# Optimization experiments

Hardware: AMD Instinct MI355X
Metric: run time of the kernel (lower is better)

Reference implementation:

```python
import jax, jax.numpy as jnp
import numpy as np

EMBED_DIM = 1024
NUM_HEADS = 16
HEAD_DIM = EMBED_DIM // NUM_HEADS
QUANTUM_HEADS = 2
BATCH = 2
SEQ = 2048


def setup_inputs() -> dict:
    key = jax.random.key(0)
    ks = jax.random.split(key, 12)
    s = 1.0 / np.sqrt(EMBED_DIM)
    d = {
        "x": jax.random.normal(ks[0], (BATCH, SEQ, EMBED_DIM), jnp.float32),
        "Wq": jax.random.normal(ks[1], (EMBED_DIM, EMBED_DIM), jnp.float32) * s,
        "bq": jax.random.normal(ks[2], (EMBED_DIM,), jnp.float32) * s,
        "Wk": jax.random.normal(ks[3], (EMBED_DIM, EMBED_DIM), jnp.float32) * s,
        "bk": jax.random.normal(ks[4], (EMBED_DIM,), jnp.float32) * s,
        "Wv": jax.random.normal(ks[5], (EMBED_DIM, EMBED_DIM), jnp.float32) * s,
        "bv": jax.random.normal(ks[6], (EMBED_DIM,), jnp.float32) * s,
        "Wo": jax.random.normal(ks[7], (EMBED_DIM, EMBED_DIM), jnp.float32) * s,
        "bo": jax.random.normal(ks[8], (EMBED_DIM,), jnp.float32) * s,
        # surrogate params for the per-head quantum expectation layers
        "qw": jax.random.normal(ks[9], (QUANTUM_HEADS,), jnp.float32),
        "qb": jax.random.normal(ks[10], (QUANTUM_HEADS,), jnp.float32) * 0.1,
    }
    return d


def reference(x, Wq, bq, Wk, bk, Wv, bv, Wo, bo, qw, qb):
    B, S, E = x.shape
    H, D, QH = NUM_HEADS, HEAD_DIM, QUANTUM_HEADS

    def proj(W, b):  # nn.Linear: x @ W.T + b, then split heads -> (B,H,S,D)
        y = jnp.einsum("bse,fe->bsf", x, W) + b
        return y.reshape(B, S, H, D).transpose(0, 2, 1, 3)

    q = proj(Wq, bq)
    k = proj(Wk, bk)
    v = proj(Wv, bv)

    scores = jnp.einsum("bhsd,bhtd->bhst", q, k) / jnp.sqrt(jnp.float32(D))
    attn = jax.nn.softmax(scores, axis=-1)  # (B,H,S,S)

    # quantum-head post-softmax rescaling: per (batch, quantum head) scalar
    agg = attn[:, :QH].mean(axis=(2, 3))            # (B,QH)
    refined = jnp.cos(qw[None, :] * agg + qb[None, :])  # surrogate expectation in [-1,1]
    scale = jnp.concatenate(
        [refined, jnp.ones((B, H - QH), dtype=attn.dtype)], axis=1
    )  # (B,H)
    attn = attn * scale[:, :, None, None]

    out = jnp.einsum("bhst,bhtd->bhsd", attn, v)
    out = out.transpose(0, 2, 1, 3).reshape(B, S, E)
    out = jnp.einsum("bse,fe->bsf", out, Wo) + bo
    return out
```

## Files before the change

### kernel.cpp

```cpp
#include <hip/hip_runtime.h>
#include <hip/hip_bf16.h>

#define B_ 2
#define S_ 2048
#define E_ 1024
#define H_ 16
#define D_ 64

typedef __attribute__((ext_vector_type(8))) short short8;
typedef __attribute__((ext_vector_type(4))) float f32x4;
typedef __attribute__((ext_vector_type(16))) float f32x16;
typedef __attribute__((ext_vector_type(4))) unsigned short u16x4;

#define AS1 __attribute__((address_space(1)))
#define AS3 __attribute__((address_space(3)))

static __device__ __forceinline__ unsigned short f2bf(float f) {
  unsigned int u = __builtin_bit_cast(unsigned int, f);
  return (unsigned short)((u + 0x7fffu + ((u >> 16) & 1u)) >> 16);
}
static __device__ __forceinline__ unsigned short f2bf_f(float f) {
  unsigned int u = __builtin_bit_cast(unsigned int, f);
  return (unsigned short)((u + 0x8000u) >> 16);
}
static __device__ __forceinline__ void gload_lds16(const void* g, void* l) {
  __builtin_amdgcn_global_load_lds((const AS1 unsigned int*)g, (AS3 unsigned int*)l, 16, 0, 0);
}

__global__ __launch_bounds__(256) void cvt_all(const float* __restrict__ x,
                                               const float* __restrict__ w0,
                                               const float* __restrict__ w1,
                                               const float* __restrict__ w2,
                                               const float* __restrict__ w3,
                                               unsigned short* __restrict__ xb,
                                               unsigned short* __restrict__ wcat) {
  const int y = blockIdx.y;
  const float* src;
  unsigned short* dst;
  if (y < 4) {
    src = (y == 0) ? w0 : (y == 1) ? w1 : (y == 2) ? w2 : w3;
    dst = wcat + (size_t)y * (E_ * E_);
  } else {
    src = x + (size_t)(y - 4) * (E_ * E_);
    dst = xb + (size_t)(y - 4) * (E_ * E_);
  }
  int i = blockIdx.x * 1024 + threadIdx.x * 4;
  f32x4 v = *(const f32x4*)(src + i);
  u16x4 o;
  o.x = f2bf(v.x); o.y = f2bf(v.y); o.z = f2bf(v.z); o.w = f2bf(v.w);
  *(u16x4*)(dst + i) = o;
}

__global__ __launch_bounds__(256) void gemm_qkv3(const unsigned short* __restrict__ A,
                                                 const unsigned short* __restrict__ W,
                                                 const float* __restrict__ bq,
                                                 const float* __restrict__ bk,
                                                 const float* __restrict__ bv,
                                                 unsigned short* __restrict__ Qo,
                                                 unsigned short* __restrict__ Ko,
                                                 unsigned short* __restrict__ VT) {
  __shared__ __align__(16) unsigned short sm[128 * 64 * 2];
  unsigned short* lA = sm;
  unsigned short* lB = sm + 128 * 64;
  const int K = E_;
  const int tid  = threadIdx.x;
  const int lane = tid & 63;
  const int w    = tid >> 6;
  const int wm   = (w >> 1) * 64, wn = (w & 1) * 64;
  const int li   = lane & 15, quad = lane >> 4;
  const int e7   = li & 7;
  const int m0   = blockIdx.x * 128, n0 = blockIdx.y * 128;

  f32x4 acc[4][4];
#pragma unroll
  for (int i = 0; i < 4; ++i)
#pragma unroll
    for (int j = 0; j < 4; ++j) { f32x4 z = {0.f, 0.f, 0.f, 0.f}; acc[i][j] = z; }

  const unsigned short* pA[4];
  const unsigned short* pB[4];
#pragma unroll
  for (int q = 0; q < 4; ++q) {
    int p = tid + 256 * q, row = p >> 3, kc = (p & 7) ^ (row & 7);
    pA[q] = A + (size_t)(m0 + row) * K + kc * 8;
    pB[q] = W + (size_t)(n0 + row) * K + kc * 8;
  }

  for (int k0 = 0; k0 < K; k0 += 64) {
    __syncthreads();
#pragma unroll
    for (int q = 0; q < 4; ++q) gload_lds16(pA[q] + k0, &lA[(tid + 256 * q) * 8]);
#pragma unroll
    for (int q = 0; q < 4; ++q) gload_lds16(pB[q] + k0, &lB[(tid + 256 * q) * 8]);
    __syncthreads();
#pragma unroll
    for (int ks = 0; ks < 2; ++ks) {
      short8 af[4], bf[4];
#pragma unroll
      for (int i = 0; i < 4; ++i)
        af[i] = *(const short8*)&lA[(wm + i * 16 + li) * 64 + (((ks * 4 + quad) ^ e7) << 3)];
#pragma unroll
      for (int j = 0; j < 4; ++j)
        bf[j] = *(const short8*)&lB[(wn + j * 16 + li) * 64 + (((ks * 4 + quad) ^ e7) << 3)];
#pragma unroll
      for (int i = 0; i < 4; ++i)
#pragma unroll
        for (int j = 0; j < 4; ++j)
          acc[i][j] = __builtin_amdgcn_mfma_f32_16x16x32_bf16(af[i], bf[j], acc[i][j], 0, 0, 0);
    }
  }

  const int third = blockIdx.y >> 3;
  if (third < 2) {
    unsigned short* C = (third == 0) ? Qo : Ko;
    const float* bias = (third == 0) ? bq : bk;
    const float sc = (third == 0) ? 0.125f : 1.0f;
#pragma unroll
    for (int j = 0; j < 4; ++j) {
      int colf = (n0 & 1023) + wn + j * 16 + li;
      float bvv = bias[colf];
#pragma unroll
      for (int i = 0; i < 4; ++i)
#pragma unroll
        for (int r = 0; r < 4; ++r) {
          int row = m0 + wm + i * 16 + quad * 4 + r;
          C[(size_t)row * E_ + colf] = f2bf_f((acc[i][j][r] + bvv) * sc);
        }
    }
  } else {
    const int base = (blockIdx.y & 7) * 128;
    __syncthreads();
#pragma unroll
    for (int j = 0; j < 4; ++j) {
      int col = wn + j * 16 + li;
      float bvv = bv[base + col];
      int cm15 = col & 15;
#pragma unroll
      for (int i = 0; i < 4; ++i) {
        int s = wm + i * 16 + quad * 4;
        int off = col * 128 + (((s >> 3) ^ cm15) << 3) + (s & 7);
        u16x4 o;
        o.x = f2bf_f(acc[i][j][0] + bvv);
        o.y = f2bf_f(acc[i][j][1] + bvv);
        o.z = f2bf_f(acc[i][j][2] + bvv);
        o.w = f2bf_f(acc[i][j][3] + bvv);
        *(u16x4*)&sm[off] = o;
      }
    }
    __syncthreads();
    int col = tid >> 1, half = tid & 1;
    int colf = base + col;
    int h2 = colf >> 6, d2 = colf & 63;
    int bb = m0 >> 11, s2 = m0 & 2047;
    unsigned short* dst = VT + (((size_t)bb * 16 + h2) * 64 + d2) * 2048 + s2 + half * 64;
    int cm15 = col & 15;
#pragma unroll
    for (int u = 0; u < 8; ++u) {
      int sc2 = half * 8 + u;
      *(short8*)(dst + u * 8) = *(const short8*)&sm[col * 128 + ((sc2 ^ cm15) << 3)];
    }
  }
}

__global__ __launch_bounds__(256) void gemm_out64(const unsigned short* __restrict__ A,
                                                  const unsigned short* __restrict__ W,
                                                  const float* __restrict__ bias,
                                                  float* __restrict__ C) {
  __shared__ __align__(16) unsigned short lA[64 * 64];
  __shared__ __align__(16) unsigned short lB[128 * 64];
  const int N = E_, K = E_;
  const int tid  = threadIdx.x;
  const int lane = tid & 63;
  const int w    = tid >> 6;
  const int m0   = blockIdx.x * 64, n0 = blockIdx.y * 128;
  const int mi   = (w >> 1) * 32, ni = (w & 1) * 64;
  const int li   = lane & 15, quad = lane >> 4;
  const int e7   = li & 7;

  f32x4 acc[2][4];
#pragma unroll
  for (int i = 0; i < 2; ++i)
#pragma unroll
    for (int j = 0; j < 4; ++j) { f32x4 z = {0.f, 0.f, 0.f, 0.f}; acc[i][j] = z; }

  const unsigned short* pA[2];
  const unsigned short* pB[4];
#pragma unroll
  for (int q = 0; q < 2; ++q) {
    int p = tid + 256 * q, row = p >> 3, kc = (p & 7) ^ (row & 7);
    pA[q] = A + (size_t)(m0 + row) * K + kc * 8;
  }
#pragma unroll
  for (int q = 0; q < 4; ++q) {
    int p = tid + 256 * q, row = p >> 3, kc = (p & 7) ^ (row & 7);
    pB[q] = W + (size_t)(n0 + row) * K + kc * 8;
  }

  for (int k0 = 0; k0 < K; k0 += 64) {
    __syncthreads();
#pragma unroll
    for (int q = 0; q < 2; ++q) gload_lds16(pA[q] + k0, &lA[(tid + 256 * q) * 8]);
#pragma unroll
    for (int q = 0; q < 4; ++q) gload_lds16(pB[q] + k0, &lB[(tid + 256 * q) * 8]);
    __syncthreads();
#pragma unroll
    for (int ks = 0; ks < 2; ++ks) {
      short8 a0 = *(const short8*)&lA[(mi      + li) * 64 + (((ks * 4 + quad) ^ e7) << 3)];
      short8 a1 = *(const short8*)&lA[(mi + 16 + li) * 64 + (((ks * 4 + quad) ^ e7) << 3)];
#pragma unroll
      for (int nt = 0; nt < 4; ++nt) {
        short8 bb = *(const short8*)&lB[(ni + nt * 16 + li) * 64 + (((ks * 4 + quad) ^ e7) << 3)];
        acc[0][nt] = __builtin_amdgcn_mfma_f32_16x16x32_bf16(a0, bb, acc[0][nt], 0, 0, 0);
        acc[1][nt] = __builtin_amdgcn_mfma_f32_16x16x32_bf16(a1, bb, acc[1][nt], 0, 0, 0);
      }
    }
  }

#pragma unroll
  for (int mt = 0; mt < 2; ++mt)
#pragma unroll
    for (int nt = 0; nt < 4; ++nt) {
      int col = n0 + ni + nt * 16 + li;
      float bvv = bias[col];
#pragma unroll
      for (int r = 0; r < 4; ++r) {
        int row = m0 + mi + mt * 16 + quad * 4 + r;
        C[(size_t)row * N + col] = acc[mt][nt][r] + bvv;
      }
    }
}

__global__ __launch_bounds__(512, 4) void attn_kernel(const unsigned short* __restrict__ Q,
                                                      const unsigned short* __restrict__ Kp,
                                                      const unsigned short* __restrict__ VT,
                                                      const float* __restrict__ qw,
                                                      const float* __restrict__ qb,
                                                      unsigned short* __restrict__ O) {
  __shared__ __align__(16) char smem[81920];
  unsigned short* Qs = (unsigned short*)smem;
  unsigned short* KsB0 = (unsigned short*)(smem + 16384);
  unsigned short* VsB0 = (unsigned short*)(smem + 32768);
  unsigned short* KsB1 = (unsigned short*)(smem + 49152);
  unsigned short* VsB1 = (unsigned short*)(smem + 65536);
  float* Rbuf = (float*)(smem + 16384);
  float* Lbuf = (float*)smem;

  const int tid  = threadIdx.x;
  const int lane = tid & 63;
  const int c    = lane & 31, hi = lane >> 5;
  const int wv   = tid >> 6, wq = wv & 3, wt = wv >> 2;
  const int s0 = blockIdx.x * 128, h = blockIdx.y, b = blockIdx.z;
  const int cm7 = c & 7;

  {
    int p = tid, row = p >> 3, kc = (p & 7) ^ (row & 7);
    gload_lds16(Q + (size_t)(b * S_ + s0 + row) * E_ + h * 64 + kc * 8, &Qs[p * 8]);
    p = tid + 512; row = p >> 3; kc = (p & 7) ^ (row & 7);
    gload_lds16(Q + (size_t)(b * S_ + s0 + row) * E_ + h * 64 + kc * 8, &Qs[p * 8]);
  }
  const int kr1 = tid >> 3, kr2 = (tid + 512) >> 3;
  const unsigned short* kg1 = Kp + (size_t)(b * S_ + kr1) * E_ + h * 64 + (((tid & 7) ^ (kr1 & 7)) * 8);
  const unsigned short* kg2 = Kp + (size_t)(b * S_ + kr2) * E_ + h * 64 + ((((tid + 512) & 7) ^ (kr2 & 7)) * 8);
  const int vr1 = tid >> 4, vr2 = (tid + 512) >> 4;
  const unsigned short* vg1 = VT + ((size_t)((b * H_ + h) * 64 + vr1)) * S_ + (((tid & 15) ^ (vr1 & 7)) * 8);
  const unsigned short* vg2 = VT + ((size_t)((b * H_ + h) * 64 + vr2)) * S_ + ((((tid + 512) & 15) ^ (vr2 & 7)) * 8);

  gload_lds16(kg1, &KsB0[tid * 8]);
  gload_lds16(kg2, &KsB0[(tid + 512) * 8]);
  gload_lds16(vg1, &VsB0[tid * 8]);
  gload_lds16(vg2, &VsB0[(tid + 512) * 8]);
  kg1 += (size_t)128 * E_; kg2 += (size_t)128 * E_;
  vg1 += 128; vg2 += 128;
  __syncthreads();

  short8 qf[4];
#pragma unroll
  for (int kk = 0; kk < 4; ++kk)
    qf[kk] = *(const short8*)&Qs[(wq * 32 + c) * 64 + (((2 * kk + hi) ^ cm7) << 3)];

  f32x16 ot[2];
#pragma unroll
  for (int d = 0; d < 2; ++d)
#pragma unroll
    for (int i = 0; i < 16; ++i) ot[d][i] = 0.f;
  float lacc = 0.f;

#pragma unroll 2
  for (int tt = 0; tt < S_ / 128; ++tt) {
    if (tt < S_ / 128 - 1) {
      unsigned short* Kn = ((tt + 1) & 1) ? KsB1 : KsB0;
      unsigned short* Vn = ((tt + 1) & 1) ? VsB1 : VsB0;
      gload_lds16(kg1, &Kn[tid * 8]);
      gload_lds16(kg2, &Kn[(tid + 512) * 8]);
      gload_lds16(vg1, &Vn[tid * 8]);
      gload_lds16(vg2, &Vn[(tid + 512) * 8]);
      kg1 += (size_t)128 * E_; kg2 += (size_t)128 * E_;
      vg1 += 128; vg2 += 128;
    }
    const unsigned short* Ks = (tt & 1) ? KsB1 : KsB0;
    const unsigned short* Vs = (tt & 1) ? VsB1 : VsB0;

    f32x16 st[2];
#pragma unroll
    for (int d = 0; d < 2; ++d)
#pragma unroll
      for (int i = 0; i < 16; ++i) st[d][i] = 0.f;
#pragma unroll
    for (int tau = 0; tau < 2; ++tau) {
      const int trow = 64 * wt + 32 * tau + c;
#pragma unroll
      for (int kk = 0; kk < 4; ++kk) {
        short8 kf = *(const short8*)&Ks[trow * 64 + (((2 * kk + hi) ^ cm7) << 3)];
        st[tau] = __builtin_amdgcn_mfma_f32_32x32x16_bf16(kf, qf[kk], st[tau], 0, 0, 0);
      }
    }

    unsigned int pk[2][8];
#pragma unroll
    for (int tau = 0; tau < 2; ++tau)
#pragma unroll
      for (int m = 0; m < 4; ++m)
#pragma unroll
        for (int u = 0; u < 2; ++u) {
          float p0 = __expf(st[tau][4 * m + 2 * u]);
          float p1 = __expf(st[tau][4 * m + 2 * u + 1]);
          lacc += p0 + p1;
          pk[tau][2 * m + u] = (unsigned int)f2bf_f(p0) | ((unsigned int)f2bf_f(p1) << 16);
        }

#pragma unroll
    for (int pp = 0; pp < 2; ++pp)
#pragma unroll
      for (int tau = 0; tau < 2; ++tau) {
        unsigned int q0a = pk[tau][4 * pp + 0], q0b = pk[tau][4 * pp + 1];
        unsigned int q1a = pk[tau][4 * pp + 2], q1b = pk[tau][4 * pp + 3];
        unsigned int sa = hi ? q0a : q1a, sb = hi ? q0b : q1b;
        unsigned int ra = (unsigned int)__shfl_xor((int)sa, 32, 64);
        unsigned int rb = (unsigned int)__shfl_xor((int)sb, 32, 64);
        unsigned int oa = hi ? q1a : q0a, ob = hi ? q1b : q0b;
        unsigned int l0 = hi ? ra : oa, l1 = hi ? rb : ob;
        unsigned int h0 = hi ? oa : ra, h1 = hi ? ob : rb;
        union { unsigned int u[4]; short8 s; } bf;
        bf.u[0] = l0; bf.u[1] = l1; bf.u[2] = h0; bf.u[3] = h1;
        const int j = 2 * tau + pp;
#pragma unroll
        for (int dd = 0; dd < 2; ++dd) {
          short8 vf = *(const short8*)&Vs[(32 * dd + c) * 128 + (((8 * wt + 2 * j + hi) ^ cm7) << 3)];
          ot[dd] = __builtin_amdgcn_mfma_f32_32x32x16_bf16(vf, bf.s, ot[dd], 0, 0, 0);
        }
      }
    __syncthreads();
  }

  float l2 = lacc + __shfl_xor(lacc, 32, 64);

  if (wt == 1) {
#pragma unroll
    for (int dd = 0; dd < 2; ++dd)
#pragma unroll
      for (int i = 0; i < 16; ++i) Rbuf[(wq * 64 + lane) * 33 + dd * 16 + i] = ot[dd][i];
    Lbuf[wq * 64 + lane] = l2;
  }
  __syncthreads();
  if (wt == 0) {
    float lt = l2 + Lbuf[wq * 64 + lane];
    float scale = 1.0f;
    if (h < 2) scale = cosf(qw[h] * (1.0f / (float)S_) + qb[h]);
    float inv = scale / lt;
    const int q = s0 + wq * 32 + c;
    unsigned short* obase = O + (size_t)(b * S_ + q) * E_ + h * 64;
#pragma unroll
    for (int dd = 0; dd < 2; ++dd)
#pragma unroll
      for (int m = 0; m < 4; ++m) {
        u16x4 o;
#pragma unroll
        for (int r = 0; r < 4; ++r) {
          float v = (ot[dd][4 * m + r] + Rbuf[(wq * 64 + lane) * 33 + dd * 16 + 4 * m + r]) * inv;
          ((unsigned short*)&o)[r] = f2bf_f(v);
        }
        *(u16x4*)(obase + 32 * dd + 8 * m + 4 * hi) = o;
      }
  }
}

extern "C" void kernel_launch(void* const* d_in, const int* in_sizes, int n_in,
                              void* d_out, int out_size, void* d_ws, size_t ws_size,
                              hipStream_t stream) {
  const float* x  = (const float*)d_in[0];
  const float* Wq = (const float*)d_in[1];
  const float* bq = (const float*)d_in[2];
  const float* Wk = (const float*)d_in[3];
  const float* bk = (const float*)d_in[4];
  const float* Wv = (const float*)d_in[5];
  const float* bv = (const float*)d_in[6];
  const float* Wo = (const float*)d_in[7];
  const float* bo = (const float*)d_in[8];
  const float* qw = (const float*)d_in[9];
  const float* qb = (const float*)d_in[10];
  float* out = (float*)d_out;

  char* ws = (char*)d_ws;
  const size_t MB = 1u << 20;
  unsigned short* xb   = (unsigned short*)(ws + 0 * MB);
  unsigned short* Wcat = (unsigned short*)(ws + 8 * MB);
  unsigned short* Qb   = (unsigned short*)(ws + 16 * MB);
  unsigned short* Kb   = (unsigned short*)(ws + 24 * MB);
  unsigned short* VTb  = (unsigned short*)(ws + 32 * MB);
  unsigned short* Ob   = (unsigned short*)(ws + 40 * MB);
  unsigned short* Wob  = Wcat + (size_t)3 * E_ * E_;

  cvt_all<<<dim3(1024, 8), 256, 0, stream>>>(x, Wq, Wk, Wv, Wo, xb, Wcat);

  gemm_qkv3<<<dim3(32, 24), 256, 0, stream>>>(xb, Wcat, bq, bk, bv, Qb, Kb, VTb);

  attn_kernel<<<dim3(S_ / 128, H_, B_), 512, 0, stream>>>(Qb, Kb, VTb, qw, qb, Ob);

  gemm_out64<<<dim3(64, 8), 256, 0, stream>>>(Ob, Wob, bo, out);
}
```

Measured before the change: 201.6 us.

## Double-buffer QKV and output GEMM LDS tiles with K=32 stages

Both projection GEMMs switch from a single 64-wide K tile with two barriers per step to double-buffered 32-wide K tiles. The next tile is prefetched into LDS while MFMAs run on the current one, leaving one barrier per iteration, and the XOR swizzle is redone for the 32-element row stride. The attention kernel also packs bf16 pairs with a single byte-permute and splits the row-sum into two accumulators to shorten the dependency chain. The cost is twice as many loop iterations, each with less MFMA work to hide the barrier and load latency behind.

```diff
diff --git a/kernel.cpp b/kernel.cpp
--- a/kernel.cpp
+++ b/kernel.cpp
@@ -25,6 +25,9 @@
 }
 static __device__ __forceinline__ void gload_lds16(const void* g, void* l) {
   __builtin_amdgcn_global_load_lds((const AS1 unsigned int*)g, (AS3 unsigned int*)l, 16, 0, 0);
+}
+static __device__ __forceinline__ unsigned xswap32(unsigned x) {
+  return (unsigned)__shfl_xor((int)x, 32, 64);
 }
 
 __global__ __launch_bounds__(256) void cvt_all(const float* __restrict__ x,
@@ -59,17 +62,15 @@
                                                  unsigned short* __restrict__ Qo,
                                                  unsigned short* __restrict__ Ko,
                                                  unsigned short* __restrict__ VT) {
-  __shared__ __align__(16) unsigned short sm[128 * 64 * 2];
-  unsigned short* lA = sm;
-  unsigned short* lB = sm + 128 * 64;
+  __shared__ __align__(16) unsigned short sm[16384];
   const int K = E_;
   const int tid  = threadIdx.x;
   const int lane = tid & 63;
   const int w    = tid >> 6;
   const int wm   = (w >> 1) * 64, wn = (w & 1) * 64;
   const int li   = lane & 15, quad = lane >> 4;
-  const int e7   = li & 7;
   const int m0   = blockIdx.x * 128, n0 = blockIdx.y * 128;
+  const int kq8  = (quad ^ ((li >> 1) & 3)) << 3;
 
   f32x4 acc[4][4];
 #pragma unroll
@@ -77,37 +78,44 @@
 #pragma unroll
     for (int j = 0; j < 4; ++j) { f32x4 z = {0.f, 0.f, 0.f, 0.f}; acc[i][j] = z; }
 
-  const unsigned short* pA[4];
-  const unsigned short* pB[4];
-#pragma unroll
-  for (int q = 0; q < 4; ++q) {
-    int p = tid + 256 * q, row = p >> 3, kc = (p & 7) ^ (row & 7);
+  const unsigned short* pA[2];
+  const unsigned short* pB[2];
+#pragma unroll
+  for (int q = 0; q < 2; ++q) {
+    int p = tid + 256 * q, row = p >> 2, kc = (p & 3) ^ ((row >> 1) & 3);
     pA[q] = A + (size_t)(m0 + row) * K + kc * 8;
     pB[q] = W + (size_t)(n0 + row) * K + kc * 8;
   }
 
-  for (int k0 = 0; k0 < K; k0 += 64) {
+#define QKV_STAGE(k0, bs)                                          \
+  {                                                                \
+    unsigned short* dA = sm + (bs) * 4096;                         \
+    unsigned short* dB = sm + 8192 + (bs) * 4096;                  \
+    gload_lds16(pA[0] + (k0), &dA[tid * 8]);                       \
+    gload_lds16(pA[1] + (k0), &dA[(tid + 256) * 8]);               \
+    gload_lds16(pB[0] + (k0), &dB[tid * 8]);                       \
+    gload_lds16(pB[1] + (k0), &dB[(tid + 256) * 8]);               \
+  }
+
+  QKV_STAGE(0, 0);
+  __syncthreads();
+
+#pragma unroll 2
+  for (int kk = 0; kk < 32; ++kk) {
+    if (kk < 31) QKV_STAGE((kk + 1) * 32, (kk + 1) & 1);
+    const unsigned short* cA = sm + (kk & 1) * 4096;
+    const unsigned short* cB = sm + 8192 + (kk & 1) * 4096;
+    short8 af[4], bf[4];
+#pragma unroll
+    for (int i = 0; i < 4; ++i) af[i] = *(const short8*)&cA[(wm + i * 16 + li) * 32 + kq8];
+#pragma unroll
+    for (int j = 0; j < 4; ++j) bf[j] = *(const short8*)&cB[(wn + j * 16 + li) * 32 + kq8];
+#pragma unroll
+    for (int i = 0; i < 4; ++i)
+#pragma unroll
+      for (int j = 0; j < 4; ++j)
+        acc[i][j] = __builtin_amdgcn_mfma_f32_16x16x32_bf16(af[i], bf[j], acc[i][j], 0, 0, 0);
     __syncthreads();
-#pragma unroll
-    for (int q = 0; q < 4; ++q) gload_lds16(pA[q] + k0, &lA[(tid + 256 * q) * 8]);
-#pragma unroll
-    for (int q = 0; q < 4; ++q) gload_lds16(pB[q] + k0, &lB[(tid + 256 * q) * 8]);
-    __syncthreads();
-#pragma unroll
-    for (int ks = 0; ks < 2; ++ks) {
-      short8 af[4], bf[4];
-#pragma unroll
-      for (int i = 0; i < 4; ++i)
-        af[i] = *(const short8*)&lA[(wm + i * 16 + li) * 64 + (((ks * 4 + quad) ^ e7) << 3)];
-#pragma unroll
-      for (int j = 0; j < 4; ++j)
-        bf[j] = *(const short8*)&lB[(wn + j * 16 + li) * 64 + (((ks * 4 + quad) ^ e7) << 3)];
-#pragma unroll
-      for (int i = 0; i < 4; ++i)
-#pragma unroll
-        for (int j = 0; j < 4; ++j)
-          acc[i][j] = __builtin_amdgcn_mfma_f32_16x16x32_bf16(af[i], bf[j], acc[i][j], 0, 0, 0);
-    }
   }
 
   const int third = blockIdx.y >> 3;
@@ -129,7 +137,6 @@
     }
   } else {
     const int base = (blockIdx.y & 7) * 128;
-    __syncthreads();
 #pragma unroll
     for (int j = 0; j < 4; ++j) {
       int col = wn + j * 16 + li;
@@ -166,8 +173,7 @@
                                                   const unsigned short* __restrict__ W,
                                                   const float* __restrict__ bias,
                                                   float* __restrict__ C) {
-  __shared__ __align__(16) unsigned short lA[64 * 64];
-  __shared__ __align__(16) unsigned short lB[128 * 64];
+  __shared__ __align__(16) unsigned short sm[12288];
   const int N = E_, K = E_;
   const int tid  = threadIdx.x;
   const int lane = tid & 63;
@@ -175,7 +181,7 @@
   const int m0   = blockIdx.x * 64, n0 = blockIdx.y * 128;
   const int mi   = (w >> 1) * 32, ni = (w & 1) * 64;
   const int li   = lane & 15, quad = lane >> 4;
-  const int e7   = li & 7;
+  const int kq8  = (quad ^ ((li >> 1) & 3)) << 3;
 
   f32x4 acc[2][4];
 #pragma unroll
@@ -183,37 +189,44 @@
 #pragma unroll
     for (int j = 0; j < 4; ++j) { f32x4 z = {0.f, 0.f, 0.f, 0.f}; acc[i][j] = z; }
 
-  const unsigned short* pA[2];
-  const unsigned short* pB[4];
+  const unsigned short* pA0;
+  const unsigned short* pB[2];
+  {
+    int p = tid, row = p >> 2, kc = (p & 3) ^ ((row >> 1) & 3);
+    pA0 = A + (size_t)(m0 + row) * K + kc * 8;
+  }
 #pragma unroll
   for (int q = 0; q < 2; ++q) {
-    int p = tid + 256 * q, row = p >> 3, kc = (p & 7) ^ (row & 7);
-    pA[q] = A + (size_t)(m0 + row) * K + kc * 8;
-  }
-#pragma unroll
-  for (int q = 0; q < 4; ++q) {
-    int p = tid + 256 * q, row = p >> 3, kc = (p & 7) ^ (row & 7);
+    int p = tid + 256 * q, row = p >> 2, kc = (p & 3) ^ ((row >> 1) & 3);
     pB[q] = W + (size_t)(n0 + row) * K + kc * 8;
   }
 
-  for (int k0 = 0; k0 < K; k0 += 64) {
+#define OUT_STAGE(k0, bs)                                          \
+  {                                                                \
+    unsigned short* dA = sm + (bs) * 2048;                         \
+    unsigned short* dB = sm + 4096 + (bs) * 4096;                  \
+    gload_lds16(pA0 + (k0), &dA[tid * 8]);                         \
+    gload_lds16(pB[0] + (k0), &dB[tid * 8]);                       \
+    gload_lds16(pB[1] + (k0), &dB[(tid + 256) * 8]);               \
+  }
+
+  OUT_STAGE(0, 0);
+  __syncthreads();
+
+#pragma unroll 2
+  for (int kk = 0; kk < 32; ++kk) {
+    if (kk < 31) OUT_STAGE((kk + 1) * 32, (kk + 1) & 1);
+    const unsigned short* cA = sm + (kk & 1) * 2048;
+    const unsigned short* cB = sm + 4096 + (kk & 1) * 4096;
+    short8 a0 = *(const short8*)&cA[(mi      + li) * 32 + kq8];
+    short8 a1 = *(const short8*)&cA[(mi + 16 + li) * 32 + kq8];
+#pragma unroll
+    for (int nt = 0; nt < 4; ++nt) {
+      short8 bb = *(const short8*)&cB[(ni + nt * 16 + li) * 32 + kq8];
+      acc[0][nt] = __builtin_amdgcn_mfma_f32_16x16x32_bf16(a0, bb, acc[0][nt], 0, 0, 0);
+      acc[1][nt] = __builtin_amdgcn_mfma_f32_16x16x32_bf16(a1, bb, acc[1][nt], 0, 0, 0);
+    }
     __syncthreads();
-#pragma unroll
-    for (int q = 0; q < 2; ++q) gload_lds16(pA[q] + k0, &lA[(tid + 256 * q) * 8]);
-#pragma unroll
-    for (int q = 0; q < 4; ++q) gload_lds16(pB[q] + k0, &lB[(tid + 256 * q) * 8]);
-    __syncthreads();
-#pragma unroll
-    for (int ks = 0; ks < 2; ++ks) {
-      short8 a0 = *(const short8*)&lA[(mi      + li) * 64 + (((ks * 4 + quad) ^ e7) << 3)];
-      short8 a1 = *(const short8*)&lA[(mi + 16 + li) * 64 + (((ks * 4 + quad) ^ e7) << 3)];
-#pragma unroll
-      for (int nt = 0; nt < 4; ++nt) {
-        short8 bb = *(const short8*)&lB[(ni + nt * 16 + li) * 64 + (((ks * 4 + quad) ^ e7) << 3)];
-        acc[0][nt] = __builtin_amdgcn_mfma_f32_16x16x32_bf16(a0, bb, acc[0][nt], 0, 0, 0);
-        acc[1][nt] = __builtin_amdgcn_mfma_f32_16x16x32_bf16(a1, bb, acc[1][nt], 0, 0, 0);
-      }
-    }
   }
 
 #pragma unroll
@@ -283,7 +296,7 @@
   for (int d = 0; d < 2; ++d)
 #pragma unroll
     for (int i = 0; i < 16; ++i) ot[d][i] = 0.f;
-  float lacc = 0.f;
+  float lt0 = 0.f, lt1 = 0.f;
 
 #pragma unroll 2
   for (int tt = 0; tt < S_ / 128; ++tt) {
@@ -324,8 +337,10 @@
         for (int u = 0; u < 2; ++u) {
           float p0 = __expf(st[tau][4 * m + 2 * u]);
           float p1 = __expf(st[tau][4 * m + 2 * u + 1]);
-          lacc += p0 + p1;
-          pk[tau][2 * m + u] = (unsigned int)f2bf_f(p0) | ((unsigned int)f2bf_f(p1) << 16);
+          if (tau == 0) lt0 += p0 + p1; else lt1 += p0 + p1;
+          unsigned u0 = __builtin_bit_cast(unsigned, p0) + 0x8000u;
+          unsigned u1 = __builtin_bit_cast(unsigned, p1) + 0x8000u;
+          pk[tau][2 * m + u] = __builtin_amdgcn_perm(u1, u0, 0x07060302u);
         }
 
 #pragma unroll
@@ -335,8 +350,8 @@
         unsigned int q0a = pk[tau][4 * pp + 0], q0b = pk[tau][4 * pp + 1];
         unsigned int q1a = pk[tau][4 * pp + 2], q1b = pk[tau][4 * pp + 3];
         unsigned int sa = hi ? q0a : q1a, sb = hi ? q0b : q1b;
-        unsigned int ra = (unsigned int)__shfl_xor((int)sa, 32, 64);
-        unsigned int rb = (unsigned int)__shfl_xor((int)sb, 32, 64);
+        unsigned int ra = xswap32(sa);
+        unsigned int rb = xswap32(sb);
         unsigned int oa = hi ? q1a : q0a, ob = hi ? q1b : q0b;
         unsigned int l0 = hi ? ra : oa, l1 = hi ? rb : ob;
         unsigned int h0 = hi ? oa : ra, h1 = hi ? ob : rb;
@@ -352,6 +367,7 @@
     __syncthreads();
   }
 
+  float lacc = lt0 + lt1;
   float l2 = lacc + __shfl_xor(lacc, 32, 64);
 
   if (wt == 1) {
@@ -363,10 +379,10 @@
   }
   __syncthreads();
   if (wt == 0) {
-    float lt = l2 + Lbuf[wq * 64 + lane];
+    float ltot = l2 + Lbuf[wq * 64 + lane];
     float scale = 1.0f;
     if (h < 2) scale = cosf(qw[h] * (1.0f / (float)S_) + qb[h]);
-    float inv = scale / lt;
+    float inv = scale / ltot;
     const int q = s0 + wq * 32 + c;
     unsigned short* obase = O + (size_t)(b * S_ + q) * E_ + h * 64;
 #pragma unroll
```

New measurement: 209.3 us. +3.8%, slower.
